# Kernel optimization log

Measured on AMD Instinct MI355X. Metric: run time of the kernel, lower is better.

The kernel has to match this reference:

```python
import jax, jax.numpy as jnp
import numpy as np

EMBED_DIM = 128
N_EMBED = 10000
INPUT_SHAPE = (8, 64, 32, EMBED_DIM)


def setup_inputs() -> dict:
    key = jax.random.key(0)
    k1, k2 = jax.random.split(key)
    inputs = jax.random.normal(k1, INPUT_SHAPE, dtype=jnp.float32)
    cluster_mean = jax.random.normal(k2, (EMBED_DIM, N_EMBED), dtype=jnp.float32)
    return {"inputs": inputs, "cluster_mean": cluster_mean}


def reference(inputs, cluster_mean):
    embed_dim = cluster_mean.shape[0]
    # Flatten all leading dims: (N, D)
    samples = inputs.reshape(-1, embed_dim)
    # Squared euclidean distance to each code: (N, n_embed)
    dist = (
        jnp.sum(samples ** 2, axis=1, keepdims=True)
        - 2.0 * samples @ cluster_mean
        + jnp.sum(cluster_mean ** 2, axis=0, keepdims=True)
    )
    cluster_index = jnp.argmin(dist, axis=1).reshape(inputs.shape[:-1])
    # Embedding lookup from transposed codebook: (..., D)
    quantize = cluster_mean.T[cluster_index]
    q_loss = jnp.mean((quantize - jax.lax.stop_gradient(inputs)) ** 2)
    e_loss = jnp.mean((jax.lax.stop_gradient(quantize) - inputs) ** 2)
    loss = q_loss + 0.25 * e_loss
    # Straight-through estimator
    outputs = inputs + jax.lax.stop_gradient(quantize - inputs)
    return outputs, loss
```

## Files before the change

### kernel.cpp

```cpp
#include <hip/hip_runtime.h>

#define EMBED 128
#define NCODE 10000
#define NSAMP 16384
#define NCODE_PAD 10240
#define NSPLIT 8
#define SPLIT_CODES 1280
#define NCHUNK 20
#define CHUNK_ELEMS 8192
#define OUT_ELEMS (NSAMP * EMBED)
#define TAU 0.002f

typedef float f32x16 __attribute__((ext_vector_type(16)));
typedef short s16x8 __attribute__((ext_vector_type(8)));
typedef unsigned short ushort_t;
typedef unsigned long long u64;

#define OFF_AH  0
#define OFF_AL  2621440
#define OFF_CT  5242880
#define OFF_CN  10485760
#define OFF_KEY 10526720
#define OFF_C2  11575296
#define OFF_IDX 12099584
#define OFF_RL  12165120
#define OFF_CNT 12230656
#define OFF_BEST 12230720
#define OFF_LOSS 12361792

__device__ __forceinline__ unsigned short f2bf(float f) {
    unsigned u = __float_as_uint(f);
    return (unsigned short)((u + 0x7fffu + ((u >> 16) & 1u)) >> 16);
}
__device__ __forceinline__ float bf2f(unsigned short h) {
    return __uint_as_float(((unsigned)h) << 16);
}
__device__ __forceinline__ unsigned ordf(float f) {
    unsigned u = __float_as_uint(f);
    return (u & 0x80000000u) ? ~u : (u | 0x80000000u);
}
__device__ __forceinline__ float unordf(unsigned o) {
    return __uint_as_float((o & 0x80000000u) ? (o ^ 0x80000000u) : ~o);
}

__global__ __launch_bounds__(256) void prep_all(const float* __restrict__ C,
                                                ushort_t* __restrict__ Ah,
                                                ushort_t* __restrict__ Al,
                                                float* __restrict__ CT,
                                                float* __restrict__ cnorm,
                                                float* __restrict__ out,
                                                int* __restrict__ counter,
                                                float* __restrict__ lossbuf) {
    __shared__ float red[256];
    const int t  = threadIdx.x;
    const int nl = t & 15;
    const int kg = t >> 4;
    const int n  = blockIdx.x * 16 + nl;
    if (blockIdx.x == 0) {
        if (t == 0) { out[OUT_ELEMS] = 0.f; *counter = 0; }
        if (t < 64) lossbuf[t] = 0.f;
    }

    const int split = n / SPLIT_CODES;
    const int rem   = n % SPLIT_CODES;
    const int chunk = rem >> 6;
    const int mb    = (rem >> 5) & 1;
    const int row   = rem & 31;
    const int ks = kg >> 1, kh = kg & 1;
    const size_t eoff = (size_t)(split * NCHUNK + chunk) * CHUNK_ELEMS
                      + (size_t)(mb * 4096 + (ks * 2 + kh) * 256 + row * 8);
    const int k0 = kg * 8;
    float f[8];
    float s = 0.f;
#pragma unroll
    for (int j = 0; j < 8; ++j) {
        f[j] = (n < NCODE) ? C[(size_t)(k0 + j) * NCODE + n] : 0.f;
        s = fmaf(f[j], f[j], s);
    }
    *(float4*)(CT + (size_t)n * EMBED + k0)     = make_float4(f[0], f[1], f[2], f[3]);
    *(float4*)(CT + (size_t)n * EMBED + k0 + 4) = make_float4(f[4], f[5], f[6], f[7]);
    s16x8 vh, vl;
#pragma unroll
    for (int j = 0; j < 8; ++j) {
        unsigned short h = f2bf(f[j]);
        vh[j] = (short)h;
        vl[j] = (short)f2bf(f[j] - bf2f(h));
    }
    *(s16x8*)(Ah + eoff) = vh;
    *(s16x8*)(Al + eoff) = vl;

    red[t] = s;
    __syncthreads();
    if (t < 128) red[t] += red[t + 128];
    __syncthreads();
    if (t < 64) red[t] += red[t + 64];
    __syncthreads();
    if (t < 32) red[t] += red[t + 32];
    __syncthreads();
    if (t < 16) {
        const int nn = blockIdx.x * 16 + t;
        cnorm[nn] = (nn < NCODE) ? (red[t] + red[t + 16]) : 3.0e38f;
    }
}

__global__ __launch_bounds__(256, 2) void vq7(const float* __restrict__ X,
                                              const ushort_t* __restrict__ Ah,
                                              const ushort_t* __restrict__ Al,
                                              const float* __restrict__ cnorm,
                                              u64* __restrict__ candKey,
                                              unsigned* __restrict__ cand2) {
    __shared__ ushort_t Bs[2 * 2 * CHUNK_ELEMS];
    __shared__ float cns[SPLIT_CODES];
    const int t    = threadIdx.x;
    const int lane = t & 63;
    const int wave = t >> 6;
    const int ln   = lane & 31;
    const int kh   = lane >> 5;
    const int split = blockIdx.y;
    const int m0    = blockIdx.x * 256;
    const int sbase = split * SPLIT_CODES;

    s16x8 bh[2][8], bl[2][8];
#pragma unroll
    for (int g = 0; g < 2; ++g) {
        int m = m0 + wave * 64 + g * 32 + ln;
#pragma unroll
        for (int ks = 0; ks < 8; ++ks) {
            const float* src = X + (size_t)m * EMBED + ks * 16 + kh * 8;
            float4 f0 = *(const float4*)src;
            float4 f1 = *(const float4*)(src + 4);
            float f[8] = {f0.x, f0.y, f0.z, f0.w, f1.x, f1.y, f1.z, f1.w};
            s16x8 vh, vl;
#pragma unroll
            for (int j = 0; j < 8; ++j) {
                float v = -2.f * f[j];
                unsigned short h = f2bf(v);
                vh[j] = (short)h;
                vl[j] = (short)f2bf(v - bf2f(h));
            }
            bh[g][ks] = vh;
            bl[g][ks] = vl;
        }
    }

    for (int i = t; i < SPLIT_CODES; i += 256) cns[i] = cnorm[sbase + i];

    float v1[2] = {3.4e38f, 3.4e38f}, v2[2] = {3.4e38f, 3.4e38f};
    int   j1[2] = {0, 0};

    auto ldsw = (__attribute__((address_space(3))) ushort_t*)Bs;
    const int woff = wave * 2048;
    const size_t chbase = (size_t)(split * NCHUNK) * CHUNK_ELEMS;

    auto stage = [&](int cc, int buf) {
        const size_t sb = chbase + (size_t)cc * CHUNK_ELEMS;
        const ushort_t* sh = Ah + sb + woff + lane * 8;
        const ushort_t* sl = Al + sb + woff + lane * 8;
        const int db = buf * 2 * CHUNK_ELEMS + woff;
#pragma unroll
        for (int i = 0; i < 4; ++i) {
            __builtin_amdgcn_global_load_lds(
                (const __attribute__((address_space(1))) void*)(sh + i * 512),
                (__attribute__((address_space(3))) void*)(ldsw + db + i * 512),
                16, 0, 0);
            __builtin_amdgcn_global_load_lds(
                (const __attribute__((address_space(1))) void*)(sl + i * 512),
                (__attribute__((address_space(3))) void*)(ldsw + db + CHUNK_ELEMS + i * 512),
                16, 0, 0);
        }
    };

#define MFMA_PHASE(BB, MB, P0, P1)                                            \
    {                                                                         \
        P0 = (f32x16){0,0,0,0,0,0,0,0,0,0,0,0,0,0,0,0};                       \
        P1 = (f32x16){0,0,0,0,0,0,0,0,0,0,0,0,0,0,0,0};                       \
        _Pragma("unroll")                                                     \
        for (int ks = 0; ks < 8; ++ks) {                                      \
            const int fo = (BB) + (MB) * 4096 + (ks * 2 + kh) * 256 + ln * 8; \
            s16x8 a_h = *(const s16x8*)&Bs[fo];                               \
            s16x8 a_l = *(const s16x8*)&Bs[CHUNK_ELEMS + fo];                 \
            P0 = __builtin_amdgcn_mfma_f32_32x32x16_bf16(a_h, bh[0][ks], P0, 0, 0, 0); \
            P1 = __builtin_amdgcn_mfma_f32_32x32x16_bf16(a_h, bh[1][ks], P1, 0, 0, 0); \
            P0 = __builtin_amdgcn_mfma_f32_32x32x16_bf16(a_h, bl[0][ks], P0, 0, 0, 0); \
            P1 = __builtin_amdgcn_mfma_f32_32x32x16_bf16(a_h, bl[1][ks], P1, 0, 0, 0); \
            P0 = __builtin_amdgcn_mfma_f32_32x32x16_bf16(a_l, bh[0][ks], P0, 0, 0, 0); \
            P1 = __builtin_amdgcn_mfma_f32_32x32x16_bf16(a_l, bh[1][ks], P1, 0, 0, 0); \
        }                                                                     \
    }

#define EPI(P0, P1, CB)                                                       \
    {                                                                         \
        _Pragma("unroll")                                                     \
        for (int r = 0; r < 16; ++r) {                                        \
            const int cc = (CB) + ((r & 3) + 8 * (r >> 2));                   \
            const float cn = cns[cc];                                         \
            float d0 = P0[r] + cn;                                            \
            v2[0] = fminf(v2[0], fmaxf(d0, v1[0]));                           \
            if (d0 < v1[0]) j1[0] = cc;                                       \
            v1[0] = fminf(v1[0], d0);                                         \
            float d1 = P1[r] + cn;                                            \
            v2[1] = fminf(v2[1], fmaxf(d1, v1[1]));                           \
            if (d1 < v1[1]) j1[1] = cc;                                       \
            v1[1] = fminf(v1[1], d1);                                         \
        }                                                                     \
    }

    f32x16 aA0, aA1, aB0, aB1;
    int cbA, cbB;

    stage(0, 0);
    __syncthreads();
    {
        stage(1, 1);
        const int cb = 4 * kh;
        MFMA_PHASE(0, 0, aA0, aA1);
        cbA = cb;
        MFMA_PHASE(0, 1, aB0, aB1);
        EPI(aA0, aA1, cbA);
        cbB = cb + 32;
        __syncthreads();
    }

    for (int c = 1; c < NCHUNK; ++c) {
        const int b = c & 1;
        if (c + 1 < NCHUNK) stage(c + 1, 1 - b);
        const int bb = b * 2 * CHUNK_ELEMS;
        const int cb = c * 64 + 4 * kh;

        MFMA_PHASE(bb, 0, aA0, aA1);
        EPI(aB0, aB1, cbB);
        cbA = cb;
        MFMA_PHASE(bb, 1, aB0, aB1);
        EPI(aA0, aA1, cbA);
        cbB = cb + 32;
        __syncthreads();
    }
    EPI(aB0, aB1, cbB);

#pragma unroll
    for (int g = 0; g < 2; ++g) {
        float ov1 = __shfl_xor(v1[g], 32, 64);
        int   oj1 = __shfl_xor(j1[g], 32, 64);
        float ov2 = __shfl_xor(v2[g], 32, 64);
        float hi = fmaxf(v1[g], ov1);
        v2[g] = fminf(fminf(v2[g], ov2), hi);
        if (ov1 < v1[g] || (ov1 == v1[g] && oj1 < j1[g])) { v1[g] = ov1; j1[g] = oj1; }
        if (kh == 0) {
            int m = m0 + wave * 64 + g * 32 + ln;
            candKey[(size_t)m * NSPLIT + split] =
                ((u64)ordf(v1[g]) << 32) | (unsigned)(sbase + j1[g]);
            cand2[(size_t)m * NSPLIT + split] = ordf(v2[g]);
        }
    }
#undef MFMA_PHASE
#undef EPI
}

__global__ __launch_bounds__(256) void outfin_k(const float* __restrict__ X,
                                                const float* __restrict__ CT,
                                                const u64* __restrict__ candKey,
                                                const unsigned* __restrict__ cand2,
                                                int* __restrict__ idxf,
                                                int* __restrict__ rlist,
                                                int* __restrict__ counter,
                                                u64* __restrict__ wsBest,
                                                float* __restrict__ lossbuf,
                                                float* __restrict__ out) {
    __shared__ float red[4];
    const int t = threadIdx.x;
    const int m = blockIdx.x * 8 + (t >> 5);
    const int l = t & 31;

    int code = 0;
    if (l == 0) {
        u64 best = 0xffffffffffffffffull;
        float v2 = 3.4e38f;
#pragma unroll
        for (int s = 0; s < NSPLIT; ++s) {
            u64 k = candKey[(size_t)m * NSPLIT + s];
            unsigned o2 = cand2[(size_t)m * NSPLIT + s];
            if (k < best) {
                if (best != 0xffffffffffffffffull)
                    v2 = fminf(v2, unordf((unsigned)(best >> 32)));
                best = k;
                v2 = fminf(v2, unordf(o2));
            } else {
                v2 = fminf(v2, unordf((unsigned)(k >> 32)));
            }
        }
        code = (int)(unsigned)(best & 0xffffffffu);
        idxf[m] = code;
        float v1 = unordf((unsigned)(best >> 32));
        if (v2 - v1 <= TAU) {
            const float thr = v1 + TAU;
            int mask = 0;
#pragma unroll
            for (int s = 0; s < NSPLIT; ++s) {
                float v1s = unordf((unsigned)(candKey[(size_t)m * NSPLIT + s] >> 32));
                mask |= (v1s <= thr) ? (1 << s) : 0;
            }
            rlist[atomicAdd(counter, 1)] = m | (mask << 16);
            wsBest[m] = 0xffffffffffffffffull;
        }
    }
    code = __shfl(code, 0, 32);

    float4 q = *(const float4*)(CT + (size_t)code * EMBED + l * 4);
    float4 x = *(const float4*)(X + (size_t)m * EMBED + l * 4);
    *(float4*)(out + (size_t)m * EMBED + l * 4) = q;
    float dx = q.x - x.x, dy = q.y - x.y, dz = q.z - x.z, dw = q.w - x.w;
    float lsum = dx * dx + dy * dy + dz * dz + dw * dw;
#pragma unroll
    for (int off = 1; off < 64; off <<= 1) lsum += __shfl_xor(lsum, off, 64);
    if ((t & 63) == 0) red[t >> 6] = lsum;
    __syncthreads();
    if (t == 0)
        atomicAdd(&lossbuf[blockIdx.x & 63],
                  (red[0] + red[1] + red[2] + red[3]) * (1.25f / (float)OUT_ELEMS));
}

__global__ __launch_bounds__(256) void rescue_seg(const float* __restrict__ X,
                                                  const float* __restrict__ CT,
                                                  const float* __restrict__ cnorm,
                                                  const int* __restrict__ rlist,
                                                  const int* __restrict__ counter,
                                                  u64* __restrict__ wsBest) {
    __shared__ float xs[EMBED];
    __shared__ u64 wk[4];
    const int t = threadIdx.x;
    const int lane = t & 63;
    const int wave = t >> 6;
    const int hw = t & 31;
    const int slot = t >> 5;
    const int cnt = *counter;
    const int nw = cnt * 16;

    for (int w = blockIdx.x; w < nw; w += gridDim.x) {
        const int e  = w >> 4;
        const int sp = (w >> 1) & 7;
        const int hf = w & 1;
        const int packed = rlist[e];
        if (!((packed >> (16 + sp)) & 1)) continue;
        const int m = packed & 0xffff;
        __syncthreads();
        if (t < 32) {
            float4 v = *(const float4*)(X + (size_t)m * EMBED + t * 4);
            xs[t * 4 + 0] = v.x; xs[t * 4 + 1] = v.y;
            xs[t * 4 + 2] = v.z; xs[t * 4 + 3] = v.w;
        }
        __syncthreads();
        const float x0 = xs[hw * 4 + 0], x1 = xs[hw * 4 + 1];
        const float x2 = xs[hw * 4 + 2], x3 = xs[hw * 4 + 3];
        const int base = sp * SPLIT_CODES + hf * 640;
        u64 bk = 0xffffffffffffffffull;
        for (int it = 0; it < 20; ++it) {
            const int r0 = base + it * 32 + slot * 4;
            float4 c0 = *(const float4*)(CT + (size_t)(r0 + 0) * EMBED + hw * 4);
            float4 c1 = *(const float4*)(CT + (size_t)(r0 + 1) * EMBED + hw * 4);
            float4 c2 = *(const float4*)(CT + (size_t)(r0 + 2) * EMBED + hw * 4);
            float4 c3 = *(const float4*)(CT + (size_t)(r0 + 3) * EMBED + hw * 4);
            float p0 = x0 * c0.x, p1 = x0 * c1.x, p2 = x0 * c2.x, p3 = x0 * c3.x;
            p0 = fmaf(x1, c0.y, p0); p1 = fmaf(x1, c1.y, p1);
            p2 = fmaf(x1, c2.y, p2); p3 = fmaf(x1, c3.y, p3);
            p0 = fmaf(x2, c0.z, p0); p1 = fmaf(x2, c1.z, p1);
            p2 = fmaf(x2, c2.z, p2); p3 = fmaf(x2, c3.z, p3);
            p0 = fmaf(x3, c0.w, p0); p1 = fmaf(x3, c1.w, p1);
            p2 = fmaf(x3, c2.w, p2); p3 = fmaf(x3, c3.w, p3);
#pragma unroll
            for (int off = 1; off < 32; off <<= 1) {
                p0 += __shfl_xor(p0, off, 32);
                p1 += __shfl_xor(p1, off, 32);
                p2 += __shfl_xor(p2, off, 32);
                p3 += __shfl_xor(p3, off, 32);
            }
            if (hw == 0) {
                u64 k;
                k = ((u64)ordf(fmaf(-2.f, p0, cnorm[r0 + 0])) << 32) | (unsigned)(r0 + 0); if (k < bk) bk = k;
                k = ((u64)ordf(fmaf(-2.f, p1, cnorm[r0 + 1])) << 32) | (unsigned)(r0 + 1); if (k < bk) bk = k;
                k = ((u64)ordf(fmaf(-2.f, p2, cnorm[r0 + 2])) << 32) | (unsigned)(r0 + 2); if (k < bk) bk = k;
                k = ((u64)ordf(fmaf(-2.f, p3, cnorm[r0 + 3])) << 32) | (unsigned)(r0 + 3); if (k < bk) bk = k;
            }
        }
#pragma unroll
        for (int off = 1; off < 64; off <<= 1) {
            u64 o = __shfl_xor(bk, off, 64);
            if (o < bk) bk = o;
        }
        if (lane == 0) wk[wave] = bk;
        __syncthreads();
        if (t == 0) {
            u64 b = wk[0];
            if (wk[1] < b) b = wk[1];
            if (wk[2] < b) b = wk[2];
            if (wk[3] < b) b = wk[3];
            atomicMin(&wsBest[m], b);
        }
    }
}

__global__ __launch_bounds__(256) void patch_k(const float* __restrict__ X,
                                               const float* __restrict__ CT,
                                               const int* __restrict__ rlist,
                                               const int* __restrict__ counter,
                                               const u64* __restrict__ wsBest,
                                               const int* __restrict__ idxf,
                                               const float* __restrict__ lossbuf,
                                               float* __restrict__ out) {
    const int t = threadIdx.x;
    const int l = t & 31, sl = t >> 5;
    if (blockIdx.x == 0 && t == 0) {
        float s = 0.f;
#pragma unroll
        for (int i = 0; i < 64; ++i) s += lossbuf[i];
        atomicAdd(out + OUT_ELEMS, s);
    }
    const int cnt = *counter;
    for (int s = blockIdx.x * 8 + sl; s < cnt; s += gridDim.x * 8) {
        int m = rlist[s] & 0xffff;
        u64 key = wsBest[m];
        int jn = (int)(unsigned)(key & 0xffffffffu);
        int jo = idxf[m];
        if (jn == jo) continue;
        float4 qn = *(const float4*)(CT + (size_t)jn * EMBED + l * 4);
        float4 qo = *(const float4*)(CT + (size_t)jo * EMBED + l * 4);
        float4 x  = *(const float4*)(X + (size_t)m * EMBED + l * 4);
        *(float4*)(out + (size_t)m * EMBED + l * 4) = qn;
        float dn = (qn.x - x.x) * (qn.x - x.x) + (qn.y - x.y) * (qn.y - x.y)
                 + (qn.z - x.z) * (qn.z - x.z) + (qn.w - x.w) * (qn.w - x.w);
        float dp = (qo.x - x.x) * (qo.x - x.x) + (qo.y - x.y) * (qo.y - x.y)
                 + (qo.z - x.z) * (qo.z - x.z) + (qo.w - x.w) * (qo.w - x.w);
        float delta = dn - dp;
#pragma unroll
        for (int off = 1; off < 32; off <<= 1) delta += __shfl_xor(delta, off, 32);
        if (l == 0)
            atomicAdd(out + OUT_ELEMS, delta * (1.25f / (float)OUT_ELEMS));
    }
}

extern "C" void kernel_launch(void* const* d_in, const int* in_sizes, int n_in,
                              void* d_out, int out_size, void* d_ws, size_t ws_size,
                              hipStream_t stream) {
    const float* X = (const float*)d_in[0];
    const float* C = (const float*)d_in[1];
    float* out = (float*)d_out;
    char* ws = (char*)d_ws;

    ushort_t* Ah = (ushort_t*)(ws + OFF_AH);
    ushort_t* Al = (ushort_t*)(ws + OFF_AL);
    float* CT    = (float*)(ws + OFF_CT);
    float* cnorm = (float*)(ws + OFF_CN);
    u64* candKey = (u64*)(ws + OFF_KEY);
    unsigned* cand2 = (unsigned*)(ws + OFF_C2);
    int* idxf    = (int*)(ws + OFF_IDX);
    int* rlist   = (int*)(ws + OFF_RL);
    int* counter = (int*)(ws + OFF_CNT);
    u64* wsBest  = (u64*)(ws + OFF_BEST);
    float* lossbuf = (float*)(ws + OFF_LOSS);

    prep_all<<<NCODE_PAD / 16, 256, 0, stream>>>(C, Ah, Al, CT, cnorm, out, counter, lossbuf);
    vq7<<<dim3(NSAMP / 256, NSPLIT), 256, 0, stream>>>(X, Ah, Al, cnorm, candKey, cand2);
    outfin_k<<<NSAMP / 8, 256, 0, stream>>>(X, CT, candKey, cand2, idxf, rlist, counter, wsBest, lossbuf, out);
    rescue_seg<<<1024, 256, 0, stream>>>(X, CT, cnorm, rlist, counter, wsBest);
    patch_k<<<64, 256, 0, stream>>>(X, CT, rlist, counter, wsBest, idxf, lossbuf, out);
}
```

Before: 222.3 us.

## Fuse rescue search and patch into one kernel with per-sample blocks

Merges the rescue and patch kernels so that one block handles one ambiguous sample across all flagged splits. The block reduces the best code locally and patches the output and loss directly, with no global atomicMin. This drops one kernel launch along with the wsBest buffer and its initialisation and readback. In exchange, each block now processes a whole sample's masked splits sequentially (up to 1280 codes per split), so parallelism drops when the rescue list is short.

```diff
diff --git a/kernel.cpp b/kernel.cpp
--- a/kernel.cpp
+++ b/kernel.cpp
@@ -25,7 +25,6 @@
 #define OFF_IDX 12099584
 #define OFF_RL  12165120
 #define OFF_CNT 12230656
-#define OFF_BEST 12230720
 #define OFF_LOSS 12361792
 
 __device__ __forceinline__ unsigned short f2bf(float f) {
@@ -263,7 +262,6 @@
                                                 int* __restrict__ idxf,
                                                 int* __restrict__ rlist,
                                                 int* __restrict__ counter,
-                                                u64* __restrict__ wsBest,
                                                 float* __restrict__ lossbuf,
                                                 float* __restrict__ out) {
     __shared__ float red[4];
@@ -300,7 +298,6 @@
                 mask |= (v1s <= thr) ? (1 << s) : 0;
             }
             rlist[atomicAdd(counter, 1)] = m | (mask << 16);
-            wsBest[m] = 0xffffffffffffffffull;
         }
     }
     code = __shfl(code, 0, 32);
@@ -319,29 +316,34 @@
                   (red[0] + red[1] + red[2] + red[3]) * (1.25f / (float)OUT_ELEMS));
 }
 
-__global__ __launch_bounds__(256) void rescue_seg(const float* __restrict__ X,
-                                                  const float* __restrict__ CT,
-                                                  const float* __restrict__ cnorm,
-                                                  const int* __restrict__ rlist,
-                                                  const int* __restrict__ counter,
-                                                  u64* __restrict__ wsBest) {
+__global__ __launch_bounds__(256) void rescue2(const float* __restrict__ X,
+                                               const float* __restrict__ CT,
+                                               const float* __restrict__ cnorm,
+                                               const int* __restrict__ rlist,
+                                               const int* __restrict__ counter,
+                                               const int* __restrict__ idxf,
+                                               const float* __restrict__ lossbuf,
+                                               float* __restrict__ out) {
     __shared__ float xs[EMBED];
     __shared__ u64 wk[4];
+    __shared__ int jn_sh;
     const int t = threadIdx.x;
     const int lane = t & 63;
     const int wave = t >> 6;
     const int hw = t & 31;
     const int slot = t >> 5;
+    if (blockIdx.x == 0 && t == 0) {
+        float s = 0.f;
+#pragma unroll
+        for (int i = 0; i < 64; ++i) s += lossbuf[i];
+        atomicAdd(out + OUT_ELEMS, s);
+    }
     const int cnt = *counter;
-    const int nw = cnt * 16;
-
-    for (int w = blockIdx.x; w < nw; w += gridDim.x) {
-        const int e  = w >> 4;
-        const int sp = (w >> 1) & 7;
-        const int hf = w & 1;
+
+    for (int e = blockIdx.x; e < cnt; e += gridDim.x) {
         const int packed = rlist[e];
-        if (!((packed >> (16 + sp)) & 1)) continue;
-        const int m = packed & 0xffff;
+        const int m    = packed & 0xffff;
+        const int mask = (packed >> 16) & 0xff;
         __syncthreads();
         if (t < 32) {
             float4 v = *(const float4*)(X + (size_t)m * EMBED + t * 4);
@@ -351,34 +353,37 @@
         __syncthreads();
         const float x0 = xs[hw * 4 + 0], x1 = xs[hw * 4 + 1];
         const float x2 = xs[hw * 4 + 2], x3 = xs[hw * 4 + 3];
-        const int base = sp * SPLIT_CODES + hf * 640;
         u64 bk = 0xffffffffffffffffull;
-        for (int it = 0; it < 20; ++it) {
-            const int r0 = base + it * 32 + slot * 4;
-            float4 c0 = *(const float4*)(CT + (size_t)(r0 + 0) * EMBED + hw * 4);
-            float4 c1 = *(const float4*)(CT + (size_t)(r0 + 1) * EMBED + hw * 4);
-            float4 c2 = *(const float4*)(CT + (size_t)(r0 + 2) * EMBED + hw * 4);
-            float4 c3 = *(const float4*)(CT + (size_t)(r0 + 3) * EMBED + hw * 4);
-            float p0 = x0 * c0.x, p1 = x0 * c1.x, p2 = x0 * c2.x, p3 = x0 * c3.x;
-            p0 = fmaf(x1, c0.y, p0); p1 = fmaf(x1, c1.y, p1);
-            p2 = fmaf(x1, c2.y, p2); p3 = fmaf(x1, c3.y, p3);
-            p0 = fmaf(x2, c0.z, p0); p1 = fmaf(x2, c1.z, p1);
-            p2 = fmaf(x2, c2.z, p2); p3 = fmaf(x2, c3.z, p3);
-            p0 = fmaf(x3, c0.w, p0); p1 = fmaf(x3, c1.w, p1);
-            p2 = fmaf(x3, c2.w, p2); p3 = fmaf(x3, c3.w, p3);
-#pragma unroll
-            for (int off = 1; off < 32; off <<= 1) {
-                p0 += __shfl_xor(p0, off, 32);
-                p1 += __shfl_xor(p1, off, 32);
-                p2 += __shfl_xor(p2, off, 32);
-                p3 += __shfl_xor(p3, off, 32);
-            }
-            if (hw == 0) {
-                u64 k;
-                k = ((u64)ordf(fmaf(-2.f, p0, cnorm[r0 + 0])) << 32) | (unsigned)(r0 + 0); if (k < bk) bk = k;
-                k = ((u64)ordf(fmaf(-2.f, p1, cnorm[r0 + 1])) << 32) | (unsigned)(r0 + 1); if (k < bk) bk = k;
-                k = ((u64)ordf(fmaf(-2.f, p2, cnorm[r0 + 2])) << 32) | (unsigned)(r0 + 2); if (k < bk) bk = k;
-                k = ((u64)ordf(fmaf(-2.f, p3, cnorm[r0 + 3])) << 32) | (unsigned)(r0 + 3); if (k < bk) bk = k;
+        for (int sp = 0; sp < NSPLIT; ++sp) {
+            if (!((mask >> sp) & 1)) continue;
+            const int base = sp * SPLIT_CODES;
+            for (int it = 0; it < 40; ++it) {
+                const int r0 = base + it * 32 + slot * 4;
+                float4 c0 = *(const float4*)(CT + (size_t)(r0 + 0) * EMBED + hw * 4);
+                float4 c1 = *(const float4*)(CT + (size_t)(r0 + 1) * EMBED + hw * 4);
+                float4 c2 = *(const float4*)(CT + (size_t)(r0 + 2) * EMBED + hw * 4);
+                float4 c3 = *(const float4*)(CT + (size_t)(r0 + 3) * EMBED + hw * 4);
+                float p0 = x0 * c0.x, p1 = x0 * c1.x, p2 = x0 * c2.x, p3 = x0 * c3.x;
+                p0 = fmaf(x1, c0.y, p0); p1 = fmaf(x1, c1.y, p1);
+                p2 = fmaf(x1, c2.y, p2); p3 = fmaf(x1, c3.y, p3);
+                p0 = fmaf(x2, c0.z, p0); p1 = fmaf(x2, c1.z, p1);
+                p2 = fmaf(x2, c2.z, p2); p3 = fmaf(x2, c3.z, p3);
+                p0 = fmaf(x3, c0.w, p0); p1 = fmaf(x3, c1.w, p1);
+                p2 = fmaf(x3, c2.w, p2); p3 = fmaf(x3, c3.w, p3);
+#pragma unroll
+                for (int off = 1; off < 32; off <<= 1) {
+                    p0 += __shfl_xor(p0, off, 32);
+                    p1 += __shfl_xor(p1, off, 32);
+                    p2 += __shfl_xor(p2, off, 32);
+                    p3 += __shfl_xor(p3, off, 32);
+                }
+                if (hw == 0) {
+                    u64 k;
+                    k = ((u64)ordf(fmaf(-2.f, p0, cnorm[r0 + 0])) << 32) | (unsigned)(r0 + 0); if (k < bk) bk = k;
+                    k = ((u64)ordf(fmaf(-2.f, p1, cnorm[r0 + 1])) << 32) | (unsigned)(r0 + 1); if (k < bk) bk = k;
+                    k = ((u64)ordf(fmaf(-2.f, p2, cnorm[r0 + 2])) << 32) | (unsigned)(r0 + 2); if (k < bk) bk = k;
+                    k = ((u64)ordf(fmaf(-2.f, p3, cnorm[r0 + 3])) << 32) | (unsigned)(r0 + 3); if (k < bk) bk = k;
+                }
             }
         }
 #pragma unroll
@@ -393,47 +398,27 @@
             if (wk[1] < b) b = wk[1];
             if (wk[2] < b) b = wk[2];
             if (wk[3] < b) b = wk[3];
-            atomicMin(&wsBest[m], b);
-        }
-    }
-}
-
-__global__ __launch_bounds__(256) void patch_k(const float* __restrict__ X,
-                                               const float* __restrict__ CT,
-                                               const int* __restrict__ rlist,
-                                               const int* __restrict__ counter,
-                                               const u64* __restrict__ wsBest,
-                                               const int* __restrict__ idxf,
-                                               const float* __restrict__ lossbuf,
-                                               float* __restrict__ out) {
-    const int t = threadIdx.x;
-    const int l = t & 31, sl = t >> 5;
-    if (blockIdx.x == 0 && t == 0) {
-        float s = 0.f;
-#pragma unroll
-        for (int i = 0; i < 64; ++i) s += lossbuf[i];
-        atomicAdd(out + OUT_ELEMS, s);
-    }
-    const int cnt = *counter;
-    for (int s = blockIdx.x * 8 + sl; s < cnt; s += gridDim.x * 8) {
-        int m = rlist[s] & 0xffff;
-        u64 key = wsBest[m];
-        int jn = (int)(unsigned)(key & 0xffffffffu);
-        int jo = idxf[m];
-        if (jn == jo) continue;
-        float4 qn = *(const float4*)(CT + (size_t)jn * EMBED + l * 4);
-        float4 qo = *(const float4*)(CT + (size_t)jo * EMBED + l * 4);
-        float4 x  = *(const float4*)(X + (size_t)m * EMBED + l * 4);
-        *(float4*)(out + (size_t)m * EMBED + l * 4) = qn;
-        float dn = (qn.x - x.x) * (qn.x - x.x) + (qn.y - x.y) * (qn.y - x.y)
-                 + (qn.z - x.z) * (qn.z - x.z) + (qn.w - x.w) * (qn.w - x.w);
-        float dp = (qo.x - x.x) * (qo.x - x.x) + (qo.y - x.y) * (qo.y - x.y)
-                 + (qo.z - x.z) * (qo.z - x.z) + (qo.w - x.w) * (qo.w - x.w);
-        float delta = dn - dp;
-#pragma unroll
-        for (int off = 1; off < 32; off <<= 1) delta += __shfl_xor(delta, off, 32);
-        if (l == 0)
-            atomicAdd(out + OUT_ELEMS, delta * (1.25f / (float)OUT_ELEMS));
+            jn_sh = (int)(unsigned)(b & 0xffffffffu);
+        }
+        __syncthreads();
+        const int jn = jn_sh;
+        const int jo = idxf[m];
+        if (jn != jo && t < 32) {
+            const int l = t;
+            float4 qn = *(const float4*)(CT + (size_t)jn * EMBED + l * 4);
+            float4 qo = *(const float4*)(CT + (size_t)jo * EMBED + l * 4);
+            float4 x  = *(const float4*)(X + (size_t)m * EMBED + l * 4);
+            *(float4*)(out + (size_t)m * EMBED + l * 4) = qn;
+            float dn = (qn.x - x.x) * (qn.x - x.x) + (qn.y - x.y) * (qn.y - x.y)
+                     + (qn.z - x.z) * (qn.z - x.z) + (qn.w - x.w) * (qn.w - x.w);
+            float dp = (qo.x - x.x) * (qo.x - x.x) + (qo.y - x.y) * (qo.y - x.y)
+                     + (qo.z - x.z) * (qo.z - x.z) + (qo.w - x.w) * (qo.w - x.w);
+            float delta = dn - dp;
+#pragma unroll
+            for (int off = 1; off < 32; off <<= 1) delta += __shfl_xor(delta, off, 32);
+            if (l == 0)
+                atomicAdd(out + OUT_ELEMS, delta * (1.25f / (float)OUT_ELEMS));
+        }
     }
 }
 
@@ -454,12 +439,10 @@
     int* idxf    = (int*)(ws + OFF_IDX);
     int* rlist   = (int*)(ws + OFF_RL);
     int* counter = (int*)(ws + OFF_CNT);
-    u64* wsBest  = (u64*)(ws + OFF_BEST);
     float* lossbuf = (float*)(ws + OFF_LOSS);
 
     prep_all<<<NCODE_PAD / 16, 256, 0, stream>>>(C, Ah, Al, CT, cnorm, out, counter, lossbuf);
     vq7<<<dim3(NSAMP / 256, NSPLIT), 256, 0, stream>>>(X, Ah, Al, cnorm, candKey, cand2);
-    outfin_k<<<NSAMP / 8, 256, 0, stream>>>(X, CT, candKey, cand2, idxf, rlist, counter, wsBest, lossbuf, out);
-    rescue_seg<<<1024, 256, 0, stream>>>(X, CT, cnorm, rlist, counter, wsBest);
-    patch_k<<<64, 256, 0, stream>>>(X, CT, rlist, counter, wsBest, idxf, lossbuf, out);
-}
+    outfin_k<<<NSAMP / 8, 256, 0, stream>>>(X, CT, candKey, cand2, idxf, rlist, counter, lossbuf, out);
+    rescue2<<<1024, 256, 0, stream>>>(X, CT, cnorm, rlist, counter, idxf, lossbuf, out);
+}
```

After: 280.2 us. 26.0% more time.
